# Optimization experiments

Hardware: AMD Instinct MI355X
Metric: run time of the kernel (lower is better)

## Reference

```python
import jax, jax.numpy as jnp
import numpy as np

N, E, F, H, G, EPS = 50000, 500000, 128, 192, 256, 1e-5


def setup_inputs() -> dict:
    key = jax.random.key(0)
    ks = jax.random.split(key, 16)
    s = 0.05
    return {
        "x": jax.random.normal(ks[0], (N, F), jnp.float32),
        "edge_index": jax.random.randint(ks[1], (2, E), 0, N),
        "batch": jnp.sort(jax.random.randint(ks[2], (N,), 0, G)),
        "num_graphs": G,
        "w_rel0": jax.random.normal(ks[3], (H, F)) * s,
        "b_rel0": jnp.zeros((H,), jnp.float32),
        "w_root0": jax.random.normal(ks[4], (H, F)) * s,
        "w_rel": jax.random.normal(ks[5], (3, H, H)) * s,
        "b_rel": jnp.zeros((3, H), jnp.float32),
        "w_root": jax.random.normal(ks[6], (3, H, H)) * s,
        "bn_gamma": jnp.ones((4, H), jnp.float32),
        "bn_beta": jnp.zeros((4, H), jnp.float32),
        "head_w1": jax.random.normal(ks[7], (H, H)) * s,
        "head_b1": jnp.zeros((H,), jnp.float32),
        "head_w2": jax.random.normal(ks[8], (H, H)) * s,
        "head_b2": jnp.zeros((H,), jnp.float32),
        "out_w": jax.random.normal(ks[9], (1, H)) * s,
        "out_b": jnpp if False else jnp.zeros((1,), jnp.float32),
    }


def _conv_bn_relu(x, src, dst, n_nodes, wr, br, wroot, gamma, beta):
    # PyG GraphConv: out_i = lin_rel(sum_{j->i} x_j) + lin_root(x_i)
    agg = jax.ops.segment_sum(x[src], dst, num_segments=n_nodes)  # [N, d]
    h = agg @ wr.T + br + x @ wroot.T                             # [N, H]
    mu = h.mean(axis=0)
    var = h.var(axis=0)  # biased, as torch BN train mode
    h = (h - mu) * jax.lax.rsqrt(var + EPS) * gamma + beta
    return jax.nn.relu(h)


def reference(x, edge_index, batch, num_graphs, w_rel0, b_rel0, w_root0,
              w_rel, b_rel, w_root, bn_gamma, bn_beta,
              head_w1, head_b1, head_w2, head_b2, out_w, out_b):
    src, dst = edge_index[0], edge_index[1]
    n_nodes = x.shape[0]
    h = _conv_bn_relu(x, src, dst, n_nodes, w_rel0, b_rel0, w_root0,
                      bn_gamma[0], bn_beta[0])
    for i in range(3):
        h = _conv_bn_relu(h, src, dst, n_nodes, w_rel[i], b_rel[i], w_root[i],
                          bn_gamma[i + 1], bn_beta[i + 1])
    # global mean pool per graph
    sums = jax.ops.segment_sum(h, batch, num_segments=num_graphs)   # [G, H]
    cnts = jax.ops.segment_sum(jnp.ones((n_nodes,), h.dtype), batch,
                               num_segments=num_graphs)
    g = sums / jnp.maximum(cnts, 1.0)[:, None]
    # MLP head (dropout = eval) + output linear
    hh = jax.nn.relu(g @ head_w1.T + head_b1) @ head_w2.T + head_b2
    out = hh @ out_w.T + out_b                                      # [G, 1]
    return out[:, 0]
```

## Files before the change

### kernel.cpp

```cpp
#include <hip/hip_runtime.h>

#define HD 192
#define FD0 128
#define NG 256
#define BNEPS 1e-5f

#define STAT_S  1048576.0f
#define STAT_IS (1.0f / 1048576.0f)
#define POOL_S  65536.0f
#define POOL_IS (1.0f / 65536.0f)

typedef unsigned short u16;
typedef __attribute__((ext_vector_type(8))) short bf16x8;
typedef __attribute__((ext_vector_type(4))) float f32x4;

static inline int idiv(int a, int b) { return (a + b - 1) / b; }

__device__ __forceinline__ float b2f(u16 u) {
    unsigned int v = ((unsigned int)u) << 16;
    return __builtin_bit_cast(float, v);
}
__device__ __forceinline__ u16 f2b(float f) {
    unsigned int x = __builtin_bit_cast(unsigned int, f);
    return (u16)((x + 0x7FFFu + ((x >> 16) & 1u)) >> 16);
}

__device__ __forceinline__ void bn_params(const long long* __restrict__ statsq,
    const float* __restrict__ gamma, const float* __restrict__ beta,
    int N, int c, float& sc, float& sh)
{
    const float inv = 1.0f / (float)N;
    const float sum = (float)statsq[c] * STAT_IS;
    const float sq  = (float)statsq[HD + c] * STAT_IS;
    const float mu  = sum * inv;
    const float var = sq * inv - mu * mu;
    const float s   = gamma[c] * rsqrtf(var + BNEPS);
    sc = s; sh = beta[c] - mu * s;
}

__device__ __forceinline__ void async_cp16(const void* g, void* l) {
    __builtin_amdgcn_global_load_lds(
        (const __attribute__((address_space(1))) unsigned int*)g,
        (__attribute__((address_space(3))) unsigned int*)l, 16, 0, 0);
}

__global__ __launch_bounds__(256) void convert_bf16(const float* __restrict__ in,
                                                    u16* __restrict__ out, int n4)
{
    const int i = blockIdx.x * 256 + threadIdx.x;
    if (i >= n4) return;
    const float4 v = ((const float4*)in)[i];
    u16 o[4] = { f2b(v.x), f2b(v.y), f2b(v.z), f2b(v.w) };
    ((ushort4*)out)[i] = *(ushort4*)o;
}

__device__ __forceinline__ void pack_one(const float* __restrict__ wr,
    const float* __restrict__ wt, u16* __restrict__ out, int K, int idx)
{
    const int j  = idx & 7;
    const int t  = idx >> 3;
    const int c  = t & 15;
    const int kg = (t >> 4) & 3;
    const int rest = t >> 6;
    const int fglob = rest % 12;
    const int chunk = rest / 12;
    const int col = fglob * 16 + c;
    const int k   = chunk * 32 + kg * 8 + j;
    const float v = (k < K) ? wr[(size_t)col * K + k] : wt[(size_t)col * K + (k - K)];
    out[idx] = f2b(v);
}

__global__ __launch_bounds__(256) void pack_fuse(const float* __restrict__ wr0,
    const float* __restrict__ wt0, const float* __restrict__ w_rel,
    const float* __restrict__ w_root, const float* __restrict__ hw1,
    const float* __restrict__ hw2, u16* __restrict__ wp0,
    u16* __restrict__ wp123, float* __restrict__ w1t, float* __restrict__ w2t)
{
    const int T0 = HD * 2 * FD0;
    const int T1 = HD * 2 * HD;
    const int TW = HD * HD;
    int idx = blockIdx.x * 256 + threadIdx.x;
    if (idx < T0) { pack_one(wr0, wt0, wp0, FD0, idx); return; }
    idx -= T0;
    if (idx < 3 * T1) {
        const int li = idx / T1;
        const int r  = idx - li * T1;
        pack_one(w_rel + (size_t)li * HD * HD, w_root + (size_t)li * HD * HD,
                 wp123 + (size_t)li * T1, HD, r);
        return;
    }
    idx -= 3 * T1;
    if (idx >= 2 * TW) return;
    const float* w = (idx < TW) ? hw1 : hw2;
    float*       o = (idx < TW) ? w1t : w2t;
    const int r = (idx < TW) ? idx : idx - TW;
    const int t = r % HD, k = r / HD;
    o[r] = w[(size_t)t * HD + k];
}

__global__ __launch_bounds__(256) void hist_kernel(const int* __restrict__ dst,
                                                   int* __restrict__ deg, int E)
{
    const int e = blockIdx.x * 256 + threadIdx.x;
    if (e < E) atomicAdd(&deg[dst[e]], 1);
}

__global__ __launch_bounds__(256) void scan_partial(const int* __restrict__ deg,
                                                    int* __restrict__ psum, int N)
{
    __shared__ int s[256];
    const int t = threadIdx.x;
    const int i = blockIdx.x * 256 + t;
    s[t] = (i < N) ? deg[i] : 0;
    __syncthreads();
    for (int off = 128; off > 0; off >>= 1) {
        if (t < off) s[t] += s[t + off];
        __syncthreads();
    }
    if (t == 0) psum[blockIdx.x] = s[0];
}

__global__ __launch_bounds__(256) void scan_small(int* __restrict__ psum, int M)
{
    __shared__ int s[256];
    const int t = threadIdx.x;
    s[t] = (t < M) ? psum[t] : 0;
    __syncthreads();
    for (int off = 1; off < 256; off <<= 1) {
        const int u = (t >= off) ? s[t - off] : 0;
        __syncthreads();
        s[t] += u;
        __syncthreads();
    }
    if (t < M) psum[t] = (t == 0) ? 0 : s[t - 1];
}

__global__ __launch_bounds__(256) void scan_expand(int* __restrict__ deg,
    const int* __restrict__ psum, int* __restrict__ rowptr, int N, int E)
{
    __shared__ int s[256];
    const int t = threadIdx.x;
    const int i = blockIdx.x * 256 + t;
    const int v = (i < N) ? deg[i] : 0;
    s[t] = v;
    __syncthreads();
    for (int off = 1; off < 256; off <<= 1) {
        const int u = (t >= off) ? s[t - off] : 0;
        __syncthreads();
        s[t] += u;
        __syncthreads();
    }
    if (i < N) {
        const int base = psum[blockIdx.x] + s[t] - v;
        rowptr[i] = base;
        deg[i]    = base;
    }
    if (i == N - 1) rowptr[N] = E;
}

__global__ __launch_bounds__(256) void fill_kernel(const int* __restrict__ src,
    const int* __restrict__ dst, int* __restrict__ cursor,
    int* __restrict__ eidx, int E)
{
    const int e = blockIdx.x * 256 + threadIdx.x;
    if (e >= E) return;
    const int p = atomicAdd(&cursor[dst[e]], 1);
    eidx[p] = src[e];
}

template<int FD, bool BN>
__global__ __launch_bounds__(256) void gather_kernel(
    const u16* __restrict__ hsrc, const int* __restrict__ rowptr,
    const int* __restrict__ eidx, u16* __restrict__ aggb, int N,
    const long long* __restrict__ statsq, const float* __restrict__ gamma,
    const float* __restrict__ beta)
{
    constexpr int OCT = FD / 8;
    __shared__ float scs[FD], shs[FD];
    const int t = threadIdx.x;
    if (BN) {
        if (t < FD) {
            float sc, sh;
            bn_params(statsq, gamma, beta, N, t, sc, sh);
            scs[t] = sc; shs[t] = sh;
        }
        __syncthreads();
    }
    const int lane = t & 63;
    const int half = lane >> 5;
    const int o    = lane & 31;
    const int n    = blockIdx.x * 4 + (t >> 6);
    if (n >= N) return;
    const bool act = (o < OCT);
    const int beg = rowptr[n], end = rowptr[n + 1];

    float scr[8], shr[8];
    if (BN && act) {
#pragma unroll
        for (int i = 0; i < 8; ++i) { scr[i] = scs[o * 8 + i]; shr[i] = shs[o * 8 + i]; }
    }

    float acc[8];
#pragma unroll
    for (int i = 0; i < 8; ++i) acc[i] = 0.f;

    auto consume = [&](uint4 v) {
        const u16* pu = (const u16*)&v;
#pragma unroll
        for (int i = 0; i < 8; ++i) {
            float f = b2f(pu[i]);
            if (BN) f = fmaxf(0.f, fmaf(f, scr[i], shr[i]));
            acc[i] += f;
        }
    };

    int j = beg + half;
    for (; j + 6 < end; j += 8) {
        const int s0 = eidx[j],     s1 = eidx[j + 2];
        const int s2 = eidx[j + 4], s3 = eidx[j + 6];
        if (act) {
            const uint4 v0 = *(const uint4*)(hsrc + (size_t)s0 * FD + o * 8);
            const uint4 v1 = *(const uint4*)(hsrc + (size_t)s1 * FD + o * 8);
            const uint4 v2 = *(const uint4*)(hsrc + (size_t)s2 * FD + o * 8);
            const uint4 v3 = *(const uint4*)(hsrc + (size_t)s3 * FD + o * 8);
            consume(v0); consume(v1); consume(v2); consume(v3);
        }
    }
    for (; j < end; j += 2) {
        const int s0 = eidx[j];
        if (act) consume(*(const uint4*)(hsrc + (size_t)s0 * FD + o * 8));
    }
#pragma unroll
    for (int i = 0; i < 8; ++i) acc[i] += __shfl_xor(acc[i], 32);

    if (half == 0 && act) {
        u16 ov[8];
#pragma unroll
        for (int i = 0; i < 8; ++i) ov[i] = f2b(acc[i]);
        *(uint4*)(aggb + (size_t)n * FD + o * 8) = *(uint4*)ov;
    }
}

template<int K1, int K2, bool BN>
__global__ __launch_bounds__(512, 1) void gemm_mfma(
    const u16* __restrict__ A1, const u16* A2,
    const u16* __restrict__ Wb, const float* __restrict__ bias,
    u16* Hout, long long* __restrict__ statsq_out,
    const long long* __restrict__ statsq_in, const float* __restrict__ gamma,
    const float* __restrict__ beta, int N)
{
    constexpr int KC  = K1 + K2;
    constexpr int NC  = KC / 32;
    constexpr int NC1 = K1 / 32;
    __shared__ u16 bsh[HD * KC];
    __shared__ float scs[K2], shs[K2];

    const int tid  = threadIdx.x;
    const int wave = tid >> 6, lane = tid & 63;
    const int c = lane & 15, kg = lane >> 4;
    const int row0 = blockIdx.x * 256 + wave * 32;

    {
        constexpr int NST = (HD * KC) / (512 * 8);
        const u16* wsrc = Wb + tid * 8;
        u16* ldst = bsh + tid * 8;
#pragma unroll
        for (int i = 0; i < NST; ++i)
            async_cp16(wsrc + i * 4096, ldst + i * 4096);
    }
    if (BN) {
        if (tid < K2) {
            float sc, sh;
            bn_params(statsq_in, gamma, beta, N, tid, sc, sh);
            scs[tid] = sc; shs[tid] = sh;
        }
    }

    int arc[2];
#pragma unroll
    for (int m = 0; m < 2; ++m) {
        const int r = row0 + m * 16 + c;
        arc[m] = r < N ? r : N - 1;
    }

    f32x4 acc[2][12];
#pragma unroll
    for (int m = 0; m < 2; ++m)
#pragma unroll
        for (int f = 0; f < 12; ++f) acc[m][f] = (f32x4){0.f, 0.f, 0.f, 0.f};

    auto aload = [&](int ch, bf16x8* d) {
#pragma unroll
        for (int m = 0; m < 2; ++m) {
            const u16* p = (ch < NC1)
                ? (A1 + (size_t)arc[m] * K1 + ch * 32 + kg * 8)
                : (A2 + (size_t)arc[m] * K2 + (ch - NC1) * 32 + kg * 8);
            d[m] = *(const bf16x8*)p;
        }
    };

    bf16x8 ring[4][2];
#pragma unroll
    for (int p = 0; p < 4; ++p)
        if (p < NC) aload(p, ring[p]);

    __syncthreads();

#pragma unroll
    for (int ch = 0; ch < NC; ++ch) {
        bf16x8 a[2] = { ring[ch & 3][0], ring[ch & 3][1] };
        if (ch + 4 < NC) aload(ch + 4, ring[ch & 3]);
        if (BN && ch >= NC1) {
            const int k0 = (ch - NC1) * 32 + kg * 8;
            const float4 s0 = *(const float4*)&scs[k0];
            const float4 s1 = *(const float4*)&scs[k0 + 4];
            const float4 h0 = *(const float4*)&shs[k0];
            const float4 h1 = *(const float4*)&shs[k0 + 4];
            const float scv[8] = {s0.x,s0.y,s0.z,s0.w,s1.x,s1.y,s1.z,s1.w};
            const float shv[8] = {h0.x,h0.y,h0.z,h0.w,h1.x,h1.y,h1.z,h1.w};
#pragma unroll
            for (int m = 0; m < 2; ++m) {
                const u16* pa = (const u16*)&a[m];
                u16 tv[8];
#pragma unroll
                for (int i = 0; i < 8; ++i)
                    tv[i] = f2b(fmaxf(0.f, fmaf(b2f(pa[i]), scv[i], shv[i])));
                a[m] = *(bf16x8*)tv;
            }
        }
#pragma unroll
        for (int f = 0; f < 12; ++f) {
            const bf16x8 b = *(const bf16x8*)&bsh[ch * 6144 + f * 512 + kg * 128 + c * 8];
            acc[0][f] = __builtin_amdgcn_mfma_f32_16x16x32_bf16(a[0], b, acc[0][f], 0, 0, 0);
            acc[1][f] = __builtin_amdgcn_mfma_f32_16x16x32_bf16(a[1], b, acc[1][f], 0, 0, 0);
        }
    }

    float s1v[12], s2v[12];
#pragma unroll
    for (int f = 0; f < 12; ++f) { s1v[f] = 0.f; s2v[f] = 0.f; }

#pragma unroll
    for (int f = 0; f < 12; ++f) {
        const int col = f * 16 + c;
        const float bv = bias[col];
#pragma unroll
        for (int m = 0; m < 2; ++m)
#pragma unroll
            for (int r = 0; r < 4; ++r) {
                const int orow = row0 + m * 16 + kg * 4 + r;
                if (orow < N) {
                    const float v = acc[m][f][r] + bv;
                    s1v[f] += v;
                    s2v[f] += v * v;
                    Hout[(size_t)orow * HD + col] = f2b(v);
                }
            }
    }
#pragma unroll
    for (int f = 0; f < 12; ++f) {
        s1v[f] += __shfl_xor(s1v[f], 16); s1v[f] += __shfl_xor(s1v[f], 32);
        s2v[f] += __shfl_xor(s2v[f], 16); s2v[f] += __shfl_xor(s2v[f], 32);
    }
    __syncthreads();
    float* red = (float*)bsh;
    if (kg == 0) {
#pragma unroll
        for (int f = 0; f < 12; ++f) {
            red[wave * HD + f * 16 + c]            = s1v[f];
            red[8 * HD + wave * HD + f * 16 + c]   = s2v[f];
        }
    }
    __syncthreads();
    if (tid < HD) {
        float a1 = 0.f, a2 = 0.f;
#pragma unroll
        for (int w = 0; w < 8; ++w) {
            a1 += red[w * HD + tid];
            a2 += red[8 * HD + w * HD + tid];
        }
        atomicAdd((unsigned long long*)&statsq_out[tid],
                  (unsigned long long)(long long)llrintf(a1 * STAT_S));
        atomicAdd((unsigned long long*)&statsq_out[HD + tid],
                  (unsigned long long)(long long)llrintf(a2 * STAT_S));
    }
}

__global__ __launch_bounds__(192) void pool_partial(const u16* __restrict__ h,
    const int* __restrict__ batch, int* __restrict__ gsumq, int N,
    const long long* __restrict__ statsq, const float* __restrict__ gamma,
    const float* __restrict__ beta)
{
    __shared__ float scs[HD], shs[HD];
    const int t = threadIdx.x;
    {
        float sc, sh;
        bn_params(statsq, gamma, beta, N, t, sc, sh);
        scs[t] = sc; shs[t] = sh;
    }
    __syncthreads();
    const int rl  = t / 24;
    const int oct = t % 24;
    const int r0  = blockIdx.x * 256;
    const int rend = (r0 + 256 < N) ? r0 + 256 : N;

    float scr[8], shr[8];
#pragma unroll
    for (int i = 0; i < 8; ++i) { scr[i] = scs[oct * 8 + i]; shr[i] = shs[oct * 8 + i]; }

    float facc[8];
#pragma unroll
    for (int i = 0; i < 8; ++i) facc[i] = 0.f;
    int cur = -1;

    for (int r = r0 + rl; r < rend; r += 8) {
        const int b = batch[r];
        if (b != cur) {
            if (cur >= 0) {
                int* q = gsumq + (size_t)cur * HD + oct * 8;
#pragma unroll
                for (int i = 0; i < 8; ++i)
                    atomicAdd(&q[i], __float2int_rn(facc[i] * POOL_S));
            }
#pragma unroll
            for (int i = 0; i < 8; ++i) facc[i] = 0.f;
            cur = b;
        }
        const uint4 pv = *(const uint4*)(h + (size_t)r * HD + oct * 8);
        const u16* pu = (const u16*)&pv;
#pragma unroll
        for (int i = 0; i < 8; ++i)
            facc[i] += fmaxf(0.f, fmaf(b2f(pu[i]), scr[i], shr[i]));
    }
    if (cur >= 0) {
        int* q = gsumq + (size_t)cur * HD + oct * 8;
#pragma unroll
        for (int i = 0; i < 8; ++i)
            atomicAdd(&q[i], __float2int_rn(facc[i] * POOL_S));
    }
}

__global__ __launch_bounds__(192) void head_kernel(
    const int* __restrict__ gsumq, const int* __restrict__ batch, int N,
    const float* __restrict__ w1t, const float* __restrict__ b1,
    const float* __restrict__ w2t, const float* __restrict__ b2,
    const float* __restrict__ ow, const float* __restrict__ ob,
    float* __restrict__ out)
{
    __shared__ float gv[HD];
    __shared__ float h1[HD];
    __shared__ float h2[HD];
    const int g = blockIdx.x;
    const int t = threadIdx.x;

    int lo = 0, hi = N;
    while (lo < hi) { int m = (lo + hi) >> 1; if (batch[m] < g) lo = m + 1; else hi = m; }
    const int start = lo;
    hi = N;
    while (lo < hi) { int m = (lo + hi) >> 1; if (batch[m] < g + 1) lo = m + 1; else hi = m; }
    const int end = lo;
    const float cnt = fmaxf((float)(end - start), 1.0f);

    gv[t] = (float)gsumq[(size_t)g * HD + t] * POOL_IS / cnt;
    __syncthreads();
    {
        float acc = b1[t];
#pragma unroll 4
        for (int k = 0; k < HD; ++k)
            acc = fmaf(gv[k], w1t[k * HD + t], acc);
        h1[t] = fmaxf(acc, 0.f);
    }
    __syncthreads();
    {
        float acc = b2[t];
#pragma unroll 4
        for (int k = 0; k < HD; ++k)
            acc = fmaf(h1[k], w2t[k * HD + t], acc);
        h2[t] = acc * ow[t];
    }
    __syncthreads();
    if (t < 64) {
        float s = h2[t] + h2[t + 64] + h2[t + 128];
#pragma unroll
        for (int d = 1; d < 64; d <<= 1) s += __shfl_xor(s, d);
        if (t == 0) out[g] = s + ob[0];
    }
}

extern "C" void kernel_launch(void* const* d_in, const int* in_sizes, int n_in,
                              void* d_out, int out_size, void* d_ws, size_t ws_size,
                              hipStream_t stream)
{
    const float* x       = (const float*)d_in[0];
    const int*   ei      = (const int*)d_in[1];
    const int*   batch   = (const int*)d_in[2];
    const float* w_rel0  = (const float*)d_in[4];
    const float* b_rel0  = (const float*)d_in[5];
    const float* w_root0 = (const float*)d_in[6];
    const float* w_rel   = (const float*)d_in[7];
    const float* b_rel   = (const float*)d_in[8];
    const float* w_root  = (const float*)d_in[9];
    const float* bn_g    = (const float*)d_in[10];
    const float* bn_b    = (const float*)d_in[11];
    const float* hw1     = (const float*)d_in[12];
    const float* hb1     = (const float*)d_in[13];
    const float* hw2     = (const float*)d_in[14];
    const float* hb2     = (const float*)d_in[15];
    const float* ow      = (const float*)d_in[16];
    const float* ob      = (const float*)d_in[17];
    float* out = (float*)d_out;

    const int N = in_sizes[0] / FD0;
    const int E = in_sizes[1] / 2;
    const int* src = ei;
    const int* dst = ei + E;
    const int M = idiv(N, 256);

    char* ws = (char*)d_ws;
    size_t off = 0;
    u16*   xb   = (u16*)(ws + off);   off += (size_t)N * FD0 * 2;
    u16*   h    = (u16*)(ws + off);   off += (size_t)N * HD * 2;
    u16*   aggb = (u16*)(ws + off);   off += (size_t)N * HD * 2;
    u16*   wp0  = (u16*)(ws + off);   off += (size_t)HD * 2 * FD0 * 2;
    u16*   wp123= (u16*)(ws + off);   off += (size_t)3 * HD * 2 * HD * 2;
    off = (off + 15) & ~(size_t)15;
    float* w1t = (float*)(ws + off); off += (size_t)HD * HD * 4;
    float* w2t = (float*)(ws + off); off += (size_t)HD * HD * 4;
    long long* statsq4 = (long long*)(ws + off); off += 4 * 2 * HD * sizeof(long long);
    int*   gsumq  = (int*)(ws + off); off += (size_t)NG * HD * 4;
    int*   rowptr = (int*)(ws + off); off += (size_t)(N + 1) * 4;
    int*   deg    = (int*)(ws + off); off += (size_t)N * 4;
    int*   psum   = (int*)(ws + off); off += (size_t)M * 4;
    int*   eidx   = (int*)(ws + off); off += (size_t)E * 4;

    const dim3 b256(256), b512(512), b192(192);

    convert_bf16<<<idiv(N * FD0 / 4, 256), b256, 0, stream>>>(x, xb, N * FD0 / 4);
    pack_fuse<<<idiv(HD * 2 * FD0 + 3 * HD * 2 * HD + 2 * HD * HD, 256), b256, 0,
                stream>>>(w_rel0, w_root0, w_rel, w_root, hw1, hw2,
                          wp0, wp123, w1t, w2t);
    hipMemsetAsync(statsq4, 0, 4 * 2 * HD * sizeof(long long) + (size_t)NG * HD * 4,
                   stream);
    hipMemsetAsync(deg, 0, (size_t)N * sizeof(int), stream);
    hist_kernel<<<idiv(E, 256), b256, 0, stream>>>(dst, deg, E);
    scan_partial<<<M, b256, 0, stream>>>(deg, psum, N);
    scan_small<<<1, b256, 0, stream>>>(psum, M);
    scan_expand<<<M, b256, 0, stream>>>(deg, psum, rowptr, N, E);
    fill_kernel<<<idiv(E, 256), b256, 0, stream>>>(src, dst, deg, eidx, E);

    gather_kernel<FD0, false><<<idiv(N, 4), b256, 0, stream>>>(
        xb, rowptr, eidx, aggb, N, nullptr, nullptr, nullptr);
    gemm_mfma<FD0, FD0, false><<<idiv(N, 256), b512, 0, stream>>>(
        aggb, xb, wp0, b_rel0, h, statsq4, nullptr, nullptr, nullptr, N);

    for (int i = 0; i < 3; ++i) {
        const long long* sin  = statsq4 + (size_t)i * 2 * HD;
        long long*       sout = statsq4 + (size_t)(i + 1) * 2 * HD;
        const float* g = bn_g + (size_t)i * HD;
        const float* b = bn_b + (size_t)i * HD;
        gather_kernel<HD, true><<<idiv(N, 4), b256, 0, stream>>>(
            h, rowptr, eidx, aggb, N, sin, g, b);
        gemm_mfma<HD, HD, true><<<idiv(N, 256), b512, 0, stream>>>(
            aggb, h, wp123 + (size_t)i * HD * 2 * HD,
            b_rel + (size_t)i * HD, h, sout, sin, g, b, N);
    }

    pool_partial<<<idiv(N, 256), b192, 0, stream>>>(
        h, batch, gsumq, N, statsq4 + 3 * 2 * (size_t)HD,
        bn_g + 3 * (size_t)HD, bn_b + 3 * (size_t)HD);
    head_kernel<<<NG, b192, 0, stream>>>(gsumq, batch, N, w1t, hb1, w2t, hb2,
                                         ow, ob, out);
}
```

Baseline: 391.5 us.

## Halve GEMM block size with two-phase weight staging; specialize 128-wide gather

The MFMA GEMM now uses 256-thread blocks covering 128 rows. It stages the packed weight matrix into shared memory in two halves, synchronizing between the K halves, so each block's LDS footprint is cut in half. The intent is to let more blocks reside per CU and overlap each other's weight staging and compute. A separate first-layer gather kernel uses 8-byte loads so all 32 lanes of each half-wave are active for the 128-wide features, where previously half of them sat idle. The trade-offs are an extra mid-kernel barrier and weight restage, and twice as many blocks each re-reading the weights.

```diff
diff --git a/kernel.cpp b/kernel.cpp
--- a/kernel.cpp
+++ b/kernel.cpp
@@ -19,6 +19,12 @@
 __device__ __forceinline__ float b2f(u16 u) {
     unsigned int v = ((unsigned int)u) << 16;
     return __builtin_bit_cast(float, v);
+}
+__device__ __forceinline__ float b2f_lo(unsigned int u) {
+    return __builtin_bit_cast(float, u << 16);
+}
+__device__ __forceinline__ float b2f_hi(unsigned int u) {
+    return __builtin_bit_cast(float, u & 0xffff0000u);
 }
 __device__ __forceinline__ u16 f2b(float f) {
     unsigned int x = __builtin_bit_cast(unsigned int, f);
@@ -168,24 +174,64 @@
     eidx[p] = src[e];
 }
 
-template<int FD, bool BN>
-__global__ __launch_bounds__(256) void gather_kernel(
+__global__ __launch_bounds__(256) void gather128(
+    const u16* __restrict__ hsrc, const int* __restrict__ rowptr,
+    const int* __restrict__ eidx, u16* __restrict__ aggb, int N)
+{
+    const int t    = threadIdx.x;
+    const int lane = t & 63;
+    const int half = lane >> 5;
+    const int g    = lane & 31;
+    const int n    = blockIdx.x * 4 + (t >> 6);
+    if (n >= N) return;
+    const int beg = rowptr[n], end = rowptr[n + 1];
+
+    float acc[4] = {0.f, 0.f, 0.f, 0.f};
+
+    auto consume = [&](uint2 v) {
+        acc[0] += b2f_lo(v.x); acc[1] += b2f_hi(v.x);
+        acc[2] += b2f_lo(v.y); acc[3] += b2f_hi(v.y);
+    };
+
+    int j = beg + half;
+    for (; j + 6 < end; j += 8) {
+        const int s0 = eidx[j],     s1 = eidx[j + 2];
+        const int s2 = eidx[j + 4], s3 = eidx[j + 6];
+        const uint2 v0 = *(const uint2*)(hsrc + (size_t)s0 * FD0 + g * 4);
+        const uint2 v1 = *(const uint2*)(hsrc + (size_t)s1 * FD0 + g * 4);
+        const uint2 v2 = *(const uint2*)(hsrc + (size_t)s2 * FD0 + g * 4);
+        const uint2 v3 = *(const uint2*)(hsrc + (size_t)s3 * FD0 + g * 4);
+        consume(v0); consume(v1); consume(v2); consume(v3);
+    }
+    for (; j < end; j += 2)
+        consume(*(const uint2*)(hsrc + (size_t)eidx[j] * FD0 + g * 4));
+
+#pragma unroll
+    for (int i = 0; i < 4; ++i) acc[i] += __shfl_xor(acc[i], 32);
+
+    if (half == 0) {
+        u16 ov[4];
+#pragma unroll
+        for (int i = 0; i < 4; ++i) ov[i] = f2b(acc[i]);
+        *(uint2*)(aggb + (size_t)n * FD0 + g * 4) = *(uint2*)ov;
+    }
+}
+
+__global__ __launch_bounds__(256) void gather192(
     const u16* __restrict__ hsrc, const int* __restrict__ rowptr,
     const int* __restrict__ eidx, u16* __restrict__ aggb, int N,
     const long long* __restrict__ statsq, const float* __restrict__ gamma,
     const float* __restrict__ beta)
 {
-    constexpr int OCT = FD / 8;
-    __shared__ float scs[FD], shs[FD];
+    constexpr int OCT = HD / 8;
+    __shared__ float scs[HD], shs[HD];
     const int t = threadIdx.x;
-    if (BN) {
-        if (t < FD) {
-            float sc, sh;
-            bn_params(statsq, gamma, beta, N, t, sc, sh);
-            scs[t] = sc; shs[t] = sh;
-        }
-        __syncthreads();
-    }
+    if (t < HD) {
+        float sc, sh;
+        bn_params(statsq, gamma, beta, N, t, sc, sh);
+        scs[t] = sc; shs[t] = sh;
+    }
+    __syncthreads();
     const int lane = t & 63;
     const int half = lane >> 5;
     const int o    = lane & 31;
@@ -195,7 +241,7 @@
     const int beg = rowptr[n], end = rowptr[n + 1];
 
     float scr[8], shr[8];
-    if (BN && act) {
+    if (act) {
 #pragma unroll
         for (int i = 0; i < 8; ++i) { scr[i] = scs[o * 8 + i]; shr[i] = shs[o * 8 + i]; }
     }
@@ -207,11 +253,8 @@
     auto consume = [&](uint4 v) {
         const u16* pu = (const u16*)&v;
 #pragma unroll
-        for (int i = 0; i < 8; ++i) {
-            float f = b2f(pu[i]);
-            if (BN) f = fmaxf(0.f, fmaf(f, scr[i], shr[i]));
-            acc[i] += f;
-        }
+        for (int i = 0; i < 8; ++i)
+            acc[i] += fmaxf(0.f, fmaf(b2f(pu[i]), scr[i], shr[i]));
     };
 
     int j = beg + half;
@@ -219,16 +262,16 @@
         const int s0 = eidx[j],     s1 = eidx[j + 2];
         const int s2 = eidx[j + 4], s3 = eidx[j + 6];
         if (act) {
-            const uint4 v0 = *(const uint4*)(hsrc + (size_t)s0 * FD + o * 8);
-            const uint4 v1 = *(const uint4*)(hsrc + (size_t)s1 * FD + o * 8);
-            const uint4 v2 = *(const uint4*)(hsrc + (size_t)s2 * FD + o * 8);
-            const uint4 v3 = *(const uint4*)(hsrc + (size_t)s3 * FD + o * 8);
+            const uint4 v0 = *(const uint4*)(hsrc + (size_t)s0 * HD + o * 8);
+            const uint4 v1 = *(const uint4*)(hsrc + (size_t)s1 * HD + o * 8);
+            const uint4 v2 = *(const uint4*)(hsrc + (size_t)s2 * HD + o * 8);
+            const uint4 v3 = *(const uint4*)(hsrc + (size_t)s3 * HD + o * 8);
             consume(v0); consume(v1); consume(v2); consume(v3);
         }
     }
     for (; j < end; j += 2) {
         const int s0 = eidx[j];
-        if (act) consume(*(const uint4*)(hsrc + (size_t)s0 * FD + o * 8));
+        if (act) consume(*(const uint4*)(hsrc + (size_t)s0 * HD + o * 8));
     }
 #pragma unroll
     for (int i = 0; i < 8; ++i) acc[i] += __shfl_xor(acc[i], 32);
@@ -237,12 +280,12 @@
         u16 ov[8];
 #pragma unroll
         for (int i = 0; i < 8; ++i) ov[i] = f2b(acc[i]);
-        *(uint4*)(aggb + (size_t)n * FD + o * 8) = *(uint4*)ov;
+        *(uint4*)(aggb + (size_t)n * HD + o * 8) = *(uint4*)ov;
     }
 }
 
 template<int K1, int K2, bool BN>
-__global__ __launch_bounds__(512, 1) void gemm_mfma(
+__global__ __launch_bounds__(256, 1) void gemm_mfma(
     const u16* __restrict__ A1, const u16* A2,
     const u16* __restrict__ Wb, const float* __restrict__ bias,
     u16* Hout, long long* __restrict__ statsq_out,
@@ -251,23 +294,26 @@
 {
     constexpr int KC  = K1 + K2;
     constexpr int NC  = KC / 32;
+    constexpr int NCH = NC / 2;
     constexpr int NC1 = K1 / 32;
-    __shared__ u16 bsh[HD * KC];
+    __shared__ u16 bsh[HD * (KC / 2)];
     __shared__ float scs[K2], shs[K2];
 
     const int tid  = threadIdx.x;
     const int wave = tid >> 6, lane = tid & 63;
     const int c = lane & 15, kg = lane >> 4;
-    const int row0 = blockIdx.x * 256 + wave * 32;
-
-    {
-        constexpr int NST = (HD * KC) / (512 * 8);
-        const u16* wsrc = Wb + tid * 8;
+    const int row0 = blockIdx.x * 128 + wave * 32;
+
+    auto stage = [&](int hf) {
+        constexpr int NST = (HD * (KC / 2)) / (256 * 8);
+        const u16* wsrc = Wb + (size_t)hf * (HD * (KC / 2)) + tid * 8;
         u16* ldst = bsh + tid * 8;
 #pragma unroll
         for (int i = 0; i < NST; ++i)
-            async_cp16(wsrc + i * 4096, ldst + i * 4096);
-    }
+            async_cp16(wsrc + i * 2048, ldst + i * 2048);
+    };
+
+    stage(0);
     if (BN) {
         if (tid < K2) {
             float sc, sh;
@@ -299,17 +345,7 @@
         }
     };
 
-    bf16x8 ring[4][2];
-#pragma unroll
-    for (int p = 0; p < 4; ++p)
-        if (p < NC) aload(p, ring[p]);
-
-    __syncthreads();
-
-#pragma unroll
-    for (int ch = 0; ch < NC; ++ch) {
-        bf16x8 a[2] = { ring[ch & 3][0], ring[ch & 3][1] };
-        if (ch + 4 < NC) aload(ch + 4, ring[ch & 3]);
+    auto bn_xform = [&](int ch, bf16x8* a) {
         if (BN && ch >= NC1) {
             const int k0 = (ch - NC1) * 32 + kg * 8;
             const float4 s0 = *(const float4*)&scs[k0];
@@ -328,9 +364,40 @@
                 a[m] = *(bf16x8*)tv;
             }
         }
+    };
+
+    bf16x8 ring[4][2];
+#pragma unroll
+    for (int p = 0; p < 4; ++p)
+        if (p < NC) aload(p, ring[p]);
+
+    __syncthreads();
+
+#pragma unroll
+    for (int ch = 0; ch < NCH; ++ch) {
+        bf16x8 a[2] = { ring[ch & 3][0], ring[ch & 3][1] };
+        if (ch + 4 < NC) aload(ch + 4, ring[ch & 3]);
+        bn_xform(ch, a);
 #pragma unroll
         for (int f = 0; f < 12; ++f) {
             const bf16x8 b = *(const bf16x8*)&bsh[ch * 6144 + f * 512 + kg * 128 + c * 8];
+            acc[0][f] = __builtin_amdgcn_mfma_f32_16x16x32_bf16(a[0], b, acc[0][f], 0, 0, 0);
+            acc[1][f] = __builtin_amdgcn_mfma_f32_16x16x32_bf16(a[1], b, acc[1][f], 0, 0, 0);
+        }
+    }
+
+    __syncthreads();
+    stage(1);
+    __syncthreads();
+
+#pragma unroll
+    for (int ch = NCH; ch < NC; ++ch) {
+        bf16x8 a[2] = { ring[ch & 3][0], ring[ch & 3][1] };
+        if (ch + 4 < NC) aload(ch + 4, ring[ch & 3]);
+        bn_xform(ch, a);
+#pragma unroll
+        for (int f = 0; f < 12; ++f) {
+            const bf16x8 b = *(const bf16x8*)&bsh[(ch - NCH) * 6144 + f * 512 + kg * 128 + c * 8];
             acc[0][f] = __builtin_amdgcn_mfma_f32_16x16x32_bf16(a[0], b, acc[0][f], 0, 0, 0);
             acc[1][f] = __builtin_amdgcn_mfma_f32_16x16x32_bf16(a[1], b, acc[1][f], 0, 0, 0);
         }
@@ -368,16 +435,16 @@
 #pragma unroll
         for (int f = 0; f < 12; ++f) {
             red[wave * HD + f * 16 + c]            = s1v[f];
-            red[8 * HD + wave * HD + f * 16 + c]   = s2v[f];
+            red[4 * HD + wave * HD + f * 16 + c]   = s2v[f];
         }
     }
     __syncthreads();
     if (tid < HD) {
         float a1 = 0.f, a2 = 0.f;
 #pragma unroll
-        for (int w = 0; w < 8; ++w) {
+        for (int w = 0; w < 4; ++w) {
             a1 += red[w * HD + tid];
-            a2 += red[8 * HD + w * HD + tid];
+            a2 += red[4 * HD + w * HD + tid];
         }
         atomicAdd((unsigned long long*)&statsq_out[tid],
                   (unsigned long long)(long long)llrintf(a1 * STAT_S));
@@ -533,7 +600,7 @@
     int*   psum   = (int*)(ws + off); off += (size_t)M * 4;
     int*   eidx   = (int*)(ws + off); off += (size_t)E * 4;
 
-    const dim3 b256(256), b512(512), b192(192);
+    const dim3 b256(256), b192(192);
 
     convert_bf16<<<idiv(N * FD0 / 4, 256), b256, 0, stream>>>(x, xb, N * FD0 / 4);
     pack_fuse<<<idiv(HD * 2 * FD0 + 3 * HD * 2 * HD + 2 * HD * HD, 256), b256, 0,
@@ -548,9 +615,8 @@
     scan_expand<<<M, b256, 0, stream>>>(deg, psum, rowptr, N, E);
     fill_kernel<<<idiv(E, 256), b256, 0, stream>>>(src, dst, deg, eidx, E);
 
-    gather_kernel<FD0, false><<<idiv(N, 4), b256, 0, stream>>>(
-        xb, rowptr, eidx, aggb, N, nullptr, nullptr, nullptr);
-    gemm_mfma<FD0, FD0, false><<<idiv(N, 256), b512, 0, stream>>>(
+    gather128<<<idiv(N, 4), b256, 0, stream>>>(xb, rowptr, eidx, aggb, N);
+    gemm_mfma<FD0, FD0, false><<<idiv(N, 128), b256, 0, stream>>>(
         aggb, xb, wp0, b_rel0, h, statsq4, nullptr, nullptr, nullptr, N);
 
     for (int i = 0; i < 3; ++i) {
@@ -558,9 +624,9 @@
         long long*       sout = statsq4 + (size_t)(i + 1) * 2 * HD;
         const float* g = bn_g + (size_t)i * HD;
         const float* b = bn_b + (size_t)i * HD;
-        gather_kernel<HD, true><<<idiv(N, 4), b256, 0, stream>>>(
+        gather192<<<idiv(N, 4), b256, 0, stream>>>(
             h, rowptr, eidx, aggb, N, sin, g, b);
-        gemm_mfma<HD, HD, true><<<idiv(N, 256), b512, 0, stream>>>(
+        gemm_mfma<HD, HD, true><<<idiv(N, 128), b256, 0, stream>>>(
             aggb, h, wp123 + (size_t)i * HD * 2 * HD,
             b_rel + (size_t)i * HD, h, sout, sin, g, b, N);
     }
```

Measured after the change: 404.5 us. 3.3% more time.
